# Optimization experiments

Measured on AMD Instinct MI355X. Metric: run time of the kernel, lower is better.

Reference implementation:

```python
import jax, jax.numpy as jnp
import numpy as np

D_MODEL = 1024
N_HEADS = 16
HEAD_DIM = D_MODEL // N_HEADS


def setup_inputs() -> dict:
    key = jax.random.key(0)
    ks = jax.random.split(key, 6)
    B, S = 4, 2048
    query = jax.random.normal(ks[0], (B, S, D_MODEL), dtype=jnp.float32)
    key_value = jax.random.normal(ks[1], (B, S, D_MODEL), dtype=jnp.float32)
    scale = 1.0 / np.sqrt(D_MODEL)
    Wq = jax.random.normal(ks[2], (D_MODEL, D_MODEL), dtype=jnp.float32) * scale
    Wk = jax.random.normal(ks[3], (D_MODEL, D_MODEL), dtype=jnp.float32) * scale
    Wv = jax.random.normal(ks[4], (D_MODEL, D_MODEL), dtype=jnp.float32) * scale
    Wo = jax.random.normal(ks[5], (D_MODEL, D_MODEL), dtype=jnp.float32) * scale
    return {"query": query, "key_value": key_value, "Wq": Wq, "Wk": Wk, "Wv": Wv, "Wo": Wo}


def reference(query, key_value, Wq, Wk, Wv, Wo):
    B, S, _ = query.shape
    H, Dh = N_HEADS, HEAD_DIM
    # nn.Linear (no bias): y = x @ W.T ; then split heads -> [B, H, S, Dh]
    q = (query @ Wq.T).reshape(B, S, H, Dh).transpose(0, 2, 1, 3)
    k = (key_value @ Wk.T).reshape(B, S, H, Dh).transpose(0, 2, 1, 3)
    v = (key_value @ Wv.T).reshape(B, S, H, Dh).transpose(0, 2, 1, 3)
    scale = Dh ** -0.5
    scores = jnp.einsum("bhqd,bhkd->bhqk", q, k) * scale  # [B,H,S,S]
    causal = jnp.tril(jnp.ones((S, S), dtype=bool))  # True where allowed
    scores = jnp.where(causal, scores, -jnp.inf)
    attn = jax.nn.softmax(scores, axis=-1)
    out = jnp.einsum("bhqk,bhkd->bhqd", attn, v)  # [B,H,S,Dh]
    out = out.transpose(0, 2, 1, 3).reshape(B, S, H * Dh)
    return out @ Wo.T
```

## Files before the change

kernel.cpp:

```cpp
#include <hip/hip_runtime.h>
#include <stdint.h>

typedef unsigned short u16;
typedef __attribute__((ext_vector_type(4))) unsigned short u16x4;
typedef __attribute__((ext_vector_type(8))) unsigned short u16x8;
typedef __attribute__((ext_vector_type(8))) __bf16 bf16x8;
typedef __attribute__((ext_vector_type(2))) _Float16 half2;
typedef __attribute__((ext_vector_type(8))) _Float16 half8;
typedef __attribute__((ext_vector_type(4))) float f32x4;

#define SEQ 2048
#define DM 1024
#define NH 16
#define DH 64
#define BATCH 4
#define MROWS (BATCH * SEQ)
#define KT32 (DM / 32)

#define SC_LOG2E 0.18033688011112042f

__device__ __forceinline__ u16 f2bf(float f) {
    uint32_t u = __builtin_bit_cast(uint32_t, f);
    u += 0x7fffu + ((u >> 16) & 1u);
    return (u16)(u >> 16);
}
__device__ __forceinline__ u16 f2h(float f) {
    return __builtin_bit_cast(u16, (_Float16)f);
}
__device__ __forceinline__ half2 pkrtz(float a, float b) {
    return __builtin_bit_cast(half2, __builtin_amdgcn_cvt_pkrtz(a, b));
}

__device__ __forceinline__ void load16_lds(const void* g, void* l) {
    __builtin_amdgcn_global_load_lds(
        (const __attribute__((address_space(1))) uint32_t*)(uintptr_t)g,
        (__attribute__((address_space(3))) uint32_t*)(uintptr_t)l,
        16, 0, 0);
}

#define N4A (MROWS * DM / 4)
#define N4W (DM * DM / 4)

__device__ __forceinline__ void cvt_one(const float* src, u16* dst, int i) {
    float4 v = ((const float4*)src)[i];
    u16x4 o;
    o[0] = f2bf(v.x); o[1] = f2bf(v.y); o[2] = f2bf(v.z); o[3] = f2bf(v.w);
    *(u16x4*)(dst + (size_t)i * 4) = o;
}

__global__ void cvt_all(const float* __restrict__ q, const float* __restrict__ kv,
                        const float* __restrict__ w0, const float* __restrict__ w1,
                        const float* __restrict__ w2, const float* __restrict__ w3,
                        u16* __restrict__ dq, u16* __restrict__ dkv,
                        u16* __restrict__ dw0, u16* __restrict__ dw1,
                        u16* __restrict__ dw2, u16* __restrict__ dw3) {
    int i = blockIdx.x * 256 + threadIdx.x;
    if (i < N4A) { cvt_one(q, dq, i); return; }
    i -= N4A;
    if (i < N4A) { cvt_one(kv, dkv, i); return; }
    i -= N4A;
    int s = i >> 18;
    int l = i & (N4W - 1);
    const float* src = s == 0 ? w0 : s == 1 ? w1 : s == 2 ? w2 : w3;
    u16* dst = s == 0 ? dw0 : s == 1 ? dw1 : s == 2 ? dw2 : dw3;
    cvt_one(src, dst, l);
}

__device__ __forceinline__ void gcore(const u16* __restrict__ Ag,
                                      const u16* __restrict__ Bg,
                                      int m0, int n0, f32x4 (&acc)[4][4]) {
    __shared__ __align__(16) u16 lds[2 * 8192];
    const int t = threadIdx.x;
    const int lane = t & 63, w = t >> 6;
    const int ln = lane & 15, quad = lane >> 4;
    const int wrow = (w >> 1) * 64, wcol = (w & 1) * 64;

    auto stage = [&](int kt, int b) {
#pragma unroll
        for (int i = 0; i < 4; ++i) {
            const int u = i * 256 + t;
            const int isB = u >> 9;
            const int row = (u & 511) >> 2, c = u & 3;
            const u16* base = isB ? Bg : Ag;
            const int g0 = (isB ? n0 : m0) + row;
            load16_lds(base + (size_t)g0 * DM + kt * 32 + ((c ^ ((row >> 1) & 3)) << 3),
                       &lds[b * 8192 + u * 8]);
        }
    };
    auto rdA = [&](int b, int mi) -> bf16x8 {
        const int row = wrow + mi * 16 + ln;
        return __builtin_bit_cast(bf16x8, *(const u16x8*)&lds[
            b * 8192 + row * 32 + ((quad ^ ((row >> 1) & 3)) << 3)]);
    };
    auto rdB = [&](int b, int nj) -> bf16x8 {
        const int row = wcol + nj * 16 + ln;
        return __builtin_bit_cast(bf16x8, *(const u16x8*)&lds[
            b * 8192 + 4096 + row * 32 + ((quad ^ ((row >> 1) & 3)) << 3)]);
    };

    stage(0, 0);
    stage(1, 1);
    asm volatile("s_waitcnt vmcnt(4)" ::: "memory");
    __builtin_amdgcn_s_barrier();

    for (int kt = 0; kt < KT32; ++kt) {
        const int b = kt & 1;
        bf16x8 af[4], bf[4];
#pragma unroll
        for (int mi = 0; mi < 4; ++mi) af[mi] = rdA(b, mi);
#pragma unroll
        for (int nj = 0; nj < 4; ++nj) bf[nj] = rdB(b, nj);
        asm volatile("s_waitcnt lgkmcnt(0)" ::: "memory");
        __builtin_amdgcn_sched_barrier(0);
        __builtin_amdgcn_s_barrier();
        if (kt < KT32 - 2) stage(kt + 2, b);
        __builtin_amdgcn_s_setprio(1);
#pragma unroll
        for (int mi = 0; mi < 4; ++mi)
#pragma unroll
            for (int nj = 0; nj < 4; ++nj)
                acc[mi][nj] = __builtin_amdgcn_mfma_f32_16x16x32_bf16(
                    af[mi], bf[nj], acc[mi][nj], 0, 0, 0);
        __builtin_amdgcn_s_setprio(0);
        if (kt < KT32 - 2) { asm volatile("s_waitcnt vmcnt(4)" ::: "memory"); }
        else               { asm volatile("s_waitcnt vmcnt(0)" ::: "memory"); }
        __builtin_amdgcn_s_barrier();
    }
}

__global__ __launch_bounds__(256, 4) void qkv_gemm(const u16* __restrict__ q_bf,
                                                   const u16* __restrict__ kv_bf,
                                                   const u16* __restrict__ wq,
                                                   const u16* __restrict__ wk,
                                                   const u16* __restrict__ wv,
                                                   u16* __restrict__ Qh,
                                                   u16* __restrict__ Kh,
                                                   u16* __restrict__ Vt) {
    const int g = blockIdx.x;
    const int xcd = g & 7, l = g >> 3;
    const int mt = xcd * 8 + (l & 7);
    const int pn = l >> 3;
    const int sel = pn >> 3;
    const int m0 = mt * 128, n0 = (pn & 7) * 128;
    const u16* A = (sel == 0) ? q_bf : kv_bf;
    const u16* B = (sel == 0) ? wq : (sel == 1 ? wk : wv);

    f32x4 acc[4][4] = {};
    gcore(A, B, m0, n0, acc);

    const int t = threadIdx.x;
    const int lane = t & 63, w = t >> 6;
    const int ln = lane & 15, quad = lane >> 4;
    const int wrow = (w >> 1) * 64, wcol = (w & 1) * 64;

    if (sel == 2) {
#pragma unroll
        for (int mi = 0; mi < 4; ++mi) {
            int rowb = m0 + wrow + mi * 16 + quad * 4;
            int bb = rowb >> 11, s = rowb & 2047;
#pragma unroll
            for (int ni = 0; ni < 4; ++ni) {
                int col = n0 + wcol + ni * 16 + ln;
                int h = col >> 6, d = col & 63;
                u16x4 o;
#pragma unroll
                for (int r = 0; r < 4; ++r) o[r] = f2h(acc[mi][ni][r]);
                *(u16x4*)(Vt + ((size_t)(bb * NH + h) * DH + d) * SEQ + s) = o;
            }
        }
    } else {
        u16* C = sel ? Kh : Qh;
        const float scale = sel ? 1.0f : SC_LOG2E;
#pragma unroll
        for (int mi = 0; mi < 4; ++mi) {
            int rowb = m0 + wrow + mi * 16 + quad * 4;
#pragma unroll
            for (int ni = 0; ni < 4; ++ni) {
                int col = n0 + wcol + ni * 16 + ln;
                int h = col >> 6, d = col & 63;
#pragma unroll
                for (int r = 0; r < 4; ++r) {
                    int row = rowb + r;
                    int bb = row >> 11, s = row & 2047;
                    C[((size_t)((bb * NH + h) * SEQ + s) << 6) + d] = f2bf(acc[mi][ni][r] * scale);
                }
            }
        }
    }
}

__global__ __launch_bounds__(256, 4) void wo_gemm(const u16* __restrict__ A,
                                                  const u16* __restrict__ B,
                                                  float* __restrict__ Cout) {
    const int g = blockIdx.x;
    const int xcd = g & 7, l = g >> 3;
    const int mt = xcd * 8 + (l & 7);
    const int nt = l >> 3;
    const int m0 = mt * 128, n0 = nt * 128;

    f32x4 acc[4][4] = {};
    gcore(A, B, m0, n0, acc);

    const int t = threadIdx.x;
    const int lane = t & 63, w = t >> 6;
    const int ln = lane & 15, quad = lane >> 4;
    const int wrow = (w >> 1) * 64, wcol = (w & 1) * 64;

#pragma unroll
    for (int mi = 0; mi < 4; ++mi) {
        int rowb = m0 + wrow + mi * 16 + quad * 4;
#pragma unroll
        for (int ni = 0; ni < 4; ++ni) {
            int col = n0 + wcol + ni * 16 + ln;
#pragma unroll
            for (int r = 0; r < 4; ++r)
                Cout[(size_t)(rowb + r) * DM + col] = acc[mi][ni][r];
        }
    }
}

__global__ __launch_bounds__(256) void attn_kernel(const u16* __restrict__ Q,
                                                   const u16* __restrict__ K,
                                                   const u16* __restrict__ Vt,
                                                   u16* __restrict__ AO) {
    __shared__ __align__(16) u16 qs[128 * 64];
    __shared__ __align__(16) u16 ks[64 * 64];
    __shared__ __align__(16) u16 vs[80 * 64];

    const int t = threadIdx.x;
    const int lane = t & 63, w = t >> 6;
    const int ln = lane & 15, quad = lane >> 4;
    const int l3 = ln & 7;
    const int bi = blockIdx.x;
    const int bh = bi & 63;
    const int qraw = bi >> 6;
    const int qtile = (bh & 1) ? (15 - qraw) : qraw;
    const int q0 = qtile * 128;
    const int qw0 = q0 + w * 32;
    const int ktmax = 2 * qtile + 1;
    const u16* Qb = Q + (size_t)bh * SEQ * DH;
    const u16* Kb = K + (size_t)bh * SEQ * DH;
    const u16* Vb = Vt + (size_t)bh * DH * SEQ;
    const int b = bh >> 4, h = bh & 15;

    const int cb = t & 7;
    const int r0 = t >> 3;
    const int swc = ((cb ^ (r0 & 7)) << 3);
    const int sg = ((r0 & 12) << 1) | ((r0 & 16) >> 2) | (r0 & 3);

    if (t < 128) {
        int j = t >> 3;
        u16 hv = (j == 0) ? 0x3C00 : 0;
        u16x8 o = {hv, hv, hv, hv, hv, hv, hv, hv};
        *(u16x8*)&vs[((64 + j) << 6) | (((t & 7) ^ (j & 7)) << 3)] = o;
    }

    u16x8 qreg[4];
#pragma unroll
    for (int i = 0; i < 4; ++i)
        qreg[i] = *(const u16x8*)(Qb + (size_t)(q0 + r0 + i * 32) * DH + cb * 8);
    u16x8 kreg[2], vreg[2];
#pragma unroll
    for (int i = 0; i < 2; ++i) {
        kreg[i] = *(const u16x8*)(Kb + (size_t)(i * 32 + sg) * DH + cb * 8);
        vreg[i] = *(const u16x8*)(Vb + (size_t)(r0 + i * 32) * SEQ + cb * 8);
    }

    f32x4 oaccT[2][5] = {};

    for (int kt = 0; kt <= ktmax; ++kt) {
        const int kv0 = kt * 64;
        __syncthreads();
        if (kt == 0) {
#pragma unroll
            for (int i = 0; i < 4; ++i)
                *(u16x8*)&qs[((r0 + i * 32) << 6) | swc] = qreg[i];
        }
#pragma unroll
        for (int i = 0; i < 2; ++i) {
            *(u16x8*)&ks[((r0 + i * 32) << 6) | swc] = kreg[i];
            *(u16x8*)&vs[((r0 + i * 32) << 6) | swc] = vreg[i];
        }
        __syncthreads();
        if (kt < ktmax) {
            const int kvn = kv0 + 64;
#pragma unroll
            for (int i = 0; i < 2; ++i) {
                kreg[i] = *(const u16x8*)(Kb + (size_t)(kvn + i * 32 + sg) * DH + cb * 8);
                vreg[i] = *(const u16x8*)(Vb + (size_t)(r0 + i * 32) * SEQ + kvn + cb * 8);
            }
        }

        if (kv0 >= qw0 + 32) continue;

        f32x4 st[2][4] = {};
#pragma unroll
        for (int half = 0; half < 2; ++half) {
            const int swz = (((half * 4 + quad) ^ l3) << 3);
            bf16x8 qf0 = __builtin_bit_cast(bf16x8, *(const u16x8*)&qs[((w * 32 + ln) << 6) | swz]);
            bf16x8 qf1 = __builtin_bit_cast(bf16x8, *(const u16x8*)&qs[((w * 32 + 16 + ln) << 6) | swz]);
#pragma unroll
            for (int ms = 0; ms < 4; ++ms) {
                bf16x8 kf = __builtin_bit_cast(bf16x8, *(const u16x8*)&ks[((ms * 16 + ln) << 6) | swz]);
                st[0][ms] = __builtin_amdgcn_mfma_f32_16x16x32_bf16(kf, qf0, st[0][ms], 0, 0, 0);
                st[1][ms] = __builtin_amdgcn_mfma_f32_16x16x32_bf16(kf, qf1, st[1][ms], 0, 0, 0);
            }
        }

        half8 pf[2][2];
#pragma unroll
        for (int qt2 = 0; qt2 < 2; ++qt2) {
            const int qbase = qw0 + qt2 * 16;
            if (kv0 + 63 > qbase) {
                const int relq = qbase + ln - kv0 - quad * 8;
#pragma unroll
                for (int ms = 0; ms < 4; ++ms)
#pragma unroll
                    for (int r = 0; r < 4; ++r)
                        if ((ms >> 1) * 32 + (ms & 1) * 4 + r > relq)
                            st[qt2][ms][r] = -3e38f;
            }
#pragma unroll
            for (int c = 0; c < 2; ++c) {
                half2 p0 = pkrtz(__builtin_amdgcn_exp2f(st[qt2][2 * c][0]),
                                 __builtin_amdgcn_exp2f(st[qt2][2 * c][1]));
                half2 p1 = pkrtz(__builtin_amdgcn_exp2f(st[qt2][2 * c][2]),
                                 __builtin_amdgcn_exp2f(st[qt2][2 * c][3]));
                half2 p2 = pkrtz(__builtin_amdgcn_exp2f(st[qt2][2 * c + 1][0]),
                                 __builtin_amdgcn_exp2f(st[qt2][2 * c + 1][1]));
                half2 p3 = pkrtz(__builtin_amdgcn_exp2f(st[qt2][2 * c + 1][2]),
                                 __builtin_amdgcn_exp2f(st[qt2][2 * c + 1][3]));
                half8 v;
                v[0] = p0[0]; v[1] = p0[1]; v[2] = p1[0]; v[3] = p1[1];
                v[4] = p2[0]; v[5] = p2[1]; v[6] = p3[0]; v[7] = p3[1];
                pf[qt2][c] = v;
            }
        }

#pragma unroll
        for (int c = 0; c < 2; ++c) {
            const int off = (((c * 4 + quad) ^ l3) << 3);
#pragma unroll
            for (int nd = 0; nd < 5; ++nd) {
                half8 vf = __builtin_bit_cast(half8, *(const u16x8*)&vs[((nd * 16 + ln) << 6) | off]);
                oaccT[0][nd] = __builtin_amdgcn_mfma_f32_16x16x32_f16(vf, pf[0][c], oaccT[0][nd], 0, 0, 0);
                oaccT[1][nd] = __builtin_amdgcn_mfma_f32_16x16x32_f16(vf, pf[1][c], oaccT[1][nd], 0, 0, 0);
            }
        }
    }

#pragma unroll
    for (int qt2 = 0; qt2 < 2; ++qt2) {
        float lv = __shfl(oaccT[qt2][4][0], ln, 64);
        float linv = 1.0f / lv;
        int q = q0 + w * 32 + qt2 * 16 + ln;
        size_t base = ((size_t)(b * SEQ + q) * DM) + h * DH + quad * 4;
#pragma unroll
        for (int nd = 0; nd < 4; ++nd) {
            u16x4 o;
#pragma unroll
            for (int r = 0; r < 4; ++r) o[r] = f2bf(oaccT[qt2][nd][r] * linv);
            *(u16x4*)&AO[base + nd * 16] = o;
        }
    }
}

extern "C" void kernel_launch(void* const* d_in, const int* in_sizes, int n_in,
                              void* d_out, int out_size, void* d_ws, size_t ws_size,
                              hipStream_t stream) {
    const float* query = (const float*)d_in[0];
    const float* key_value = (const float*)d_in[1];
    const float* Wq = (const float*)d_in[2];
    const float* Wk = (const float*)d_in[3];
    const float* Wv = (const float*)d_in[4];
    const float* Wo = (const float*)d_in[5];
    float* out = (float*)d_out;

    char* ws = (char*)d_ws;
    const size_t SZ_ACT = (size_t)MROWS * DM * 2;
    const size_t SZ_W = (size_t)DM * DM * 2;
    u16* q_bf  = (u16*)(ws + 0);
    u16* kv_bf = (u16*)(ws + SZ_ACT);
    u16* wq_bf = (u16*)(ws + 2 * SZ_ACT);
    u16* wk_bf = (u16*)(ws + 2 * SZ_ACT + SZ_W);
    u16* wv_bf = (u16*)(ws + 2 * SZ_ACT + 2 * SZ_W);
    u16* wo_bf = (u16*)(ws + 2 * SZ_ACT + 3 * SZ_W);
    u16* Qh    = (u16*)(ws + 2 * SZ_ACT + 4 * SZ_W);
    u16* Kh    = (u16*)(ws + 2 * SZ_ACT + 4 * SZ_W + SZ_ACT);
    u16* Vt    = (u16*)(ws + 2 * SZ_ACT + 4 * SZ_W + 2 * SZ_ACT);
    u16* AOb   = q_bf;

    const int n4_total = 2 * N4A + 4 * N4W;
    cvt_all<<<n4_total / 256, 256, 0, stream>>>(query, key_value, Wq, Wk, Wv, Wo,
                                                q_bf, kv_bf, wq_bf, wk_bf, wv_bf, wo_bf);

    qkv_gemm<<<1536, 256, 0, stream>>>(q_bf, kv_bf, wq_bf, wk_bf, wv_bf,
                                       Qh, Kh, Vt);

    attn_kernel<<<1024, 256, 0, stream>>>(Qh, Kh, Vt, AOb);

    wo_gemm<<<512, 256, 0, stream>>>(AOb, wo_bf, out);
}
```

Baseline: 268.2 us.

## Split GEMM LDS staging into triple-buffered A and double-buffered B

Restructures the shared GEMM core's LDS pipeline. A tiles are now triple-buffered and prefetched two k-steps ahead, while B tiles are double-buffered and prefetched one step ahead. Loads are issued at the top of each iteration, which removes the mid-iteration lgkmcnt wait and the extra barrier. The cost is a larger LDS footprint (40KB vs 32KB per block), which may limit occupancy under the 4-blocks launch bound, and B now has less prefetch distance to hide latency.

```diff
diff --git a/kernel.cpp b/kernel.cpp
--- a/kernel.cpp
+++ b/kernel.cpp
@@ -69,51 +69,56 @@
 __device__ __forceinline__ void gcore(const u16* __restrict__ Ag,
                                       const u16* __restrict__ Bg,
                                       int m0, int n0, f32x4 (&acc)[4][4]) {
-    __shared__ __align__(16) u16 lds[2 * 8192];
+    __shared__ __align__(16) u16 lds[20480];
     const int t = threadIdx.x;
     const int lane = t & 63, w = t >> 6;
     const int ln = lane & 15, quad = lane >> 4;
     const int wrow = (w >> 1) * 64, wcol = (w & 1) * 64;
 
-    auto stage = [&](int kt, int b) {
-#pragma unroll
-        for (int i = 0; i < 4; ++i) {
+    auto stageA = [&](int kt, int ab) {
+#pragma unroll
+        for (int i = 0; i < 2; ++i) {
             const int u = i * 256 + t;
-            const int isB = u >> 9;
-            const int row = (u & 511) >> 2, c = u & 3;
-            const u16* base = isB ? Bg : Ag;
-            const int g0 = (isB ? n0 : m0) + row;
-            load16_lds(base + (size_t)g0 * DM + kt * 32 + ((c ^ ((row >> 1) & 3)) << 3),
-                       &lds[b * 8192 + u * 8]);
+            const int row = u >> 2, c = u & 3;
+            load16_lds(Ag + (size_t)(m0 + row) * DM + kt * 32 + ((c ^ ((row >> 1) & 3)) << 3),
+                       &lds[ab * 4096 + u * 8]);
         }
     };
-    auto rdA = [&](int b, int mi) -> bf16x8 {
+    auto stageB = [&](int kt, int bb) {
+#pragma unroll
+        for (int i = 0; i < 2; ++i) {
+            const int u = i * 256 + t;
+            const int row = u >> 2, c = u & 3;
+            load16_lds(Bg + (size_t)(n0 + row) * DM + kt * 32 + ((c ^ ((row >> 1) & 3)) << 3),
+                       &lds[12288 + bb * 4096 + u * 8]);
+        }
+    };
+    auto rdA = [&](int ab, int mi) -> bf16x8 {
         const int row = wrow + mi * 16 + ln;
         return __builtin_bit_cast(bf16x8, *(const u16x8*)&lds[
-            b * 8192 + row * 32 + ((quad ^ ((row >> 1) & 3)) << 3)]);
+            ab * 4096 + row * 32 + ((quad ^ ((row >> 1) & 3)) << 3)]);
     };
-    auto rdB = [&](int b, int nj) -> bf16x8 {
+    auto rdB = [&](int bb, int nj) -> bf16x8 {
         const int row = wcol + nj * 16 + ln;
         return __builtin_bit_cast(bf16x8, *(const u16x8*)&lds[
-            b * 8192 + 4096 + row * 32 + ((quad ^ ((row >> 1) & 3)) << 3)]);
+            12288 + bb * 4096 + row * 32 + ((quad ^ ((row >> 1) & 3)) << 3)]);
     };
 
-    stage(0, 0);
-    stage(1, 1);
-    asm volatile("s_waitcnt vmcnt(4)" ::: "memory");
+    stageB(0, 0);
+    stageA(0, 0);
+    stageA(1, 1);
+    asm volatile("s_waitcnt vmcnt(2)" ::: "memory");
     __builtin_amdgcn_s_barrier();
 
+    int aCur = 0, aN2 = 2;
     for (int kt = 0; kt < KT32; ++kt) {
-        const int b = kt & 1;
+        if (kt < KT32 - 1) stageB(kt + 1, (kt + 1) & 1);
+        if (kt < KT32 - 2) stageA(kt + 2, aN2);
         bf16x8 af[4], bf[4];
 #pragma unroll
-        for (int mi = 0; mi < 4; ++mi) af[mi] = rdA(b, mi);
-#pragma unroll
-        for (int nj = 0; nj < 4; ++nj) bf[nj] = rdB(b, nj);
-        asm volatile("s_waitcnt lgkmcnt(0)" ::: "memory");
-        __builtin_amdgcn_sched_barrier(0);
-        __builtin_amdgcn_s_barrier();
-        if (kt < KT32 - 2) stage(kt + 2, b);
+        for (int mi = 0; mi < 4; ++mi) af[mi] = rdA(aCur, mi);
+#pragma unroll
+        for (int nj = 0; nj < 4; ++nj) bf[nj] = rdB(kt & 1, nj);
         __builtin_amdgcn_s_setprio(1);
 #pragma unroll
         for (int mi = 0; mi < 4; ++mi)
@@ -122,9 +127,11 @@
                 acc[mi][nj] = __builtin_amdgcn_mfma_f32_16x16x32_bf16(
                     af[mi], bf[nj], acc[mi][nj], 0, 0, 0);
         __builtin_amdgcn_s_setprio(0);
-        if (kt < KT32 - 2) { asm volatile("s_waitcnt vmcnt(4)" ::: "memory"); }
+        if (kt < KT32 - 2) { asm volatile("s_waitcnt vmcnt(2)" ::: "memory"); }
         else               { asm volatile("s_waitcnt vmcnt(0)" ::: "memory"); }
         __builtin_amdgcn_s_barrier();
+        aCur = (aCur == 2) ? 0 : aCur + 1;
+        aN2  = (aN2 == 2) ? 0 : aN2 + 1;
     }
 }
 
```

Result: no change. 267.0 us (-0.4%).
